# Kernel tuning notes

Hardware: AMD Instinct MI355X
Metric: run time of the kernel (lower is better)

## Reference

```python
import jax, jax.numpy as jnp
import numpy as np

# Tiny fixed contraction dims: M=3^(r_1-k), K=3^k, N=3^(r_2-k) with r_1=r_2=2, k=1
M, K, N = 3, 3, 3
R_O = 2  # output tensor rank -> output trailing shape (3,)*R_O == (3,3)


def setup_inputs() -> dict:
    key = jax.random.key(0)
    k1, k2 = jax.random.split(key)
    P, B, C = 4, 8192, 128
    T1 = jax.random.normal(k1, (P, B, C, M, K), dtype=jnp.float32)
    T2 = jax.random.normal(k2, (1, B, C, K, N), dtype=jnp.float32)
    return {"T1": T1, "T2": T2}


def reference(T1, T2):
    P, B, C = T1.shape[:3]
    T1m = T1.reshape(P, B, C, M, K)
    # T2 has a broadcast path dim of size 1; drop it and broadcast via einsum
    T2m = T2.reshape(B, C, K, N)
    out = jnp.einsum('pbcik,bckj->pbcij', T1m, T2m)
    return out.reshape((P, B, C) + (3,) * R_O)
```

## Files before the change

### kernel.cpp

```cpp
#include <hip/hip_runtime.h>


typedef float floatx4 __attribute__((ext_vector_type(4)));

__global__ __launch_bounds__(256) void tc33_kernel(const float* __restrict__ T1,
                                                   const float* __restrict__ T2,
                                                   float* __restrict__ out) {
    __shared__ float so[2304];
    const long long PER_P = 9LL * 8192 * 128;
    const int tid = threadIdx.x;
    const int w = tid >> 6;
    const int l = tid & 63;
    const long long cell  = (long long)blockIdx.x * 256 + tid;
    const long long cbase = cell * 9;
    const long long wbase = (long long)blockIdx.x * 2304 + (long long)w * 576;

    float* slice = so + w * 576;
    floatx4* S4  = reinterpret_cast<floatx4*>(slice);

    float b[9];
    {
        floatx4 v0 = *reinterpret_cast<const floatx4*>(T2 + cbase);
        floatx4 v1 = *reinterpret_cast<const floatx4*>(T2 + cbase + 4);
        float   v8 = T2[cbase + 8];
        b[0] = v0.x; b[1] = v0.y; b[2] = v0.z; b[3] = v0.w;
        b[4] = v1.x; b[5] = v1.y; b[6] = v1.z; b[7] = v1.w;
        b[8] = v8;
    }

    floatx4 ra0 = *reinterpret_cast<const floatx4*>(T1 + cbase);
    floatx4 ra1 = *reinterpret_cast<const floatx4*>(T1 + cbase + 4);
    float   ra8 = T1[cbase + 8];

    #pragma unroll
    for (int p = 0; p < 4; ++p) {
        float a[9];
        a[0] = ra0.x; a[1] = ra0.y; a[2] = ra0.z; a[3] = ra0.w;
        a[4] = ra1.x; a[5] = ra1.y; a[6] = ra1.z; a[7] = ra1.w;
        a[8] = ra8;

        if (p < 3) {
            const float* An = T1 + (long long)(p + 1) * PER_P + cbase;
            ra0 = *reinterpret_cast<const floatx4*>(An);
            ra1 = *reinterpret_cast<const floatx4*>(An + 4);
            ra8 = An[8];
        }

        float o[9];
        #pragma unroll
        for (int i = 0; i < 3; ++i) {
            #pragma unroll
            for (int j = 0; j < 3; ++j) {
                float s = a[i * 3 + 0] * b[0 * 3 + j];
                s = fmaf(a[i * 3 + 1], b[1 * 3 + j], s);
                s = fmaf(a[i * 3 + 2], b[2 * 3 + j], s);
                o[i * 3 + j] = s;
            }
        }

        #pragma unroll
        for (int i = 0; i < 9; ++i) slice[l * 9 + i] = o[i];

        __builtin_amdgcn_wave_barrier();

        floatx4 s0 = S4[l];
        floatx4 s1 = S4[l + 64];
        floatx4 s2;
        if (l < 16) s2 = S4[l + 128];

        floatx4* O4 = reinterpret_cast<floatx4*>(out + (long long)p * PER_P + wbase);
        O4[l]      = s0;
        O4[l + 64] = s1;
        if (l < 16) O4[l + 128] = s2;

        __builtin_amdgcn_wave_barrier();
    }
}

extern "C" void kernel_launch(void* const* d_in, const int* in_sizes, int n_in,
                              void* d_out, int out_size, void* d_ws, size_t ws_size,
                              hipStream_t stream) {
    const float* T1 = (const float*)d_in[0];
    const float* T2 = (const float*)d_in[1];
    float* out = (float*)d_out;

    const int threads = 256;
    const int blocks = (8192 * 128) / 256;
    tc33_kernel<<<blocks, threads, 0, stream>>>(T1, T2, out);
}
```

Before: 280.7 us.

## Split path dimension across blocks instead of looping per thread

Each block now handles one (p, chunk) pair, so the grid grows from 4096 to 16384 blocks and the per-thread loop over the four path slices goes away. This gives more parallelism and more memory requests in flight with less serial work per thread. The cost is that T2 is read four times, once per path block, rather than once, though repeated reads may hit in L2 or the last-level cache. The software prefetch of the next T1 slice is also dropped.

```diff
diff --git a/kernel.cpp b/kernel.cpp
--- a/kernel.cpp
+++ b/kernel.cpp
@@ -11,70 +11,58 @@
     const int tid = threadIdx.x;
     const int w = tid >> 6;
     const int l = tid & 63;
-    const long long cell  = (long long)blockIdx.x * 256 + tid;
-    const long long cbase = cell * 9;
-    const long long wbase = (long long)blockIdx.x * 2304 + (long long)w * 576;
+    const int bid = blockIdx.x;
+    const int p = bid >> 12;
+    const int chunk = bid & 4095;
+    const long long chunkBase = (long long)chunk * 2304;
+    const long long cbase = chunkBase + tid * 9;
+    const long long abase = (long long)p * PER_P + cbase;
+    const long long wbase = (long long)p * PER_P + chunkBase + (long long)w * 576;
 
     float* slice = so + w * 576;
     floatx4* S4  = reinterpret_cast<floatx4*>(slice);
 
-    float b[9];
-    {
-        floatx4 v0 = *reinterpret_cast<const floatx4*>(T2 + cbase);
-        floatx4 v1 = *reinterpret_cast<const floatx4*>(T2 + cbase + 4);
-        float   v8 = T2[cbase + 8];
-        b[0] = v0.x; b[1] = v0.y; b[2] = v0.z; b[3] = v0.w;
-        b[4] = v1.x; b[5] = v1.y; b[6] = v1.z; b[7] = v1.w;
-        b[8] = v8;
+    floatx4 vb0 = *reinterpret_cast<const floatx4*>(T2 + cbase);
+    floatx4 vb1 = *reinterpret_cast<const floatx4*>(T2 + cbase + 4);
+    float   vb8 = T2[cbase + 8];
+    floatx4 va0 = *reinterpret_cast<const floatx4*>(T1 + abase);
+    floatx4 va1 = *reinterpret_cast<const floatx4*>(T1 + abase + 4);
+    float   va8 = T1[abase + 8];
+
+    float b[9], a[9];
+    b[0] = vb0.x; b[1] = vb0.y; b[2] = vb0.z; b[3] = vb0.w;
+    b[4] = vb1.x; b[5] = vb1.y; b[6] = vb1.z; b[7] = vb1.w;
+    b[8] = vb8;
+    a[0] = va0.x; a[1] = va0.y; a[2] = va0.z; a[3] = va0.w;
+    a[4] = va1.x; a[5] = va1.y; a[6] = va1.z; a[7] = va1.w;
+    a[8] = va8;
+
+    float o[9];
+    #pragma unroll
+    for (int i = 0; i < 3; ++i) {
+        #pragma unroll
+        for (int j = 0; j < 3; ++j) {
+            float s = a[i * 3 + 0] * b[0 * 3 + j];
+            s = fmaf(a[i * 3 + 1], b[1 * 3 + j], s);
+            s = fmaf(a[i * 3 + 2], b[2 * 3 + j], s);
+            o[i * 3 + j] = s;
+        }
     }
 
-    floatx4 ra0 = *reinterpret_cast<const floatx4*>(T1 + cbase);
-    floatx4 ra1 = *reinterpret_cast<const floatx4*>(T1 + cbase + 4);
-    float   ra8 = T1[cbase + 8];
+    #pragma unroll
+    for (int i = 0; i < 9; ++i) slice[l * 9 + i] = o[i];
 
-    #pragma unroll
-    for (int p = 0; p < 4; ++p) {
-        float a[9];
-        a[0] = ra0.x; a[1] = ra0.y; a[2] = ra0.z; a[3] = ra0.w;
-        a[4] = ra1.x; a[5] = ra1.y; a[6] = ra1.z; a[7] = ra1.w;
-        a[8] = ra8;
+    __builtin_amdgcn_wave_barrier();
 
-        if (p < 3) {
-            const float* An = T1 + (long long)(p + 1) * PER_P + cbase;
-            ra0 = *reinterpret_cast<const floatx4*>(An);
-            ra1 = *reinterpret_cast<const floatx4*>(An + 4);
-            ra8 = An[8];
-        }
+    floatx4 s0 = S4[l];
+    floatx4 s1 = S4[l + 64];
+    floatx4 s2;
+    if (l < 16) s2 = S4[l + 128];
 
-        float o[9];
-        #pragma unroll
-        for (int i = 0; i < 3; ++i) {
-            #pragma unroll
-            for (int j = 0; j < 3; ++j) {
-                float s = a[i * 3 + 0] * b[0 * 3 + j];
-                s = fmaf(a[i * 3 + 1], b[1 * 3 + j], s);
-                s = fmaf(a[i * 3 + 2], b[2 * 3 + j], s);
-                o[i * 3 + j] = s;
-            }
-        }
-
-        #pragma unroll
-        for (int i = 0; i < 9; ++i) slice[l * 9 + i] = o[i];
-
-        __builtin_amdgcn_wave_barrier();
-
-        floatx4 s0 = S4[l];
-        floatx4 s1 = S4[l + 64];
-        floatx4 s2;
-        if (l < 16) s2 = S4[l + 128];
-
-        floatx4* O4 = reinterpret_cast<floatx4*>(out + (long long)p * PER_P + wbase);
-        O4[l]      = s0;
-        O4[l + 64] = s1;
-        if (l < 16) O4[l + 128] = s2;
-
-        __builtin_amdgcn_wave_barrier();
-    }
+    floatx4* O4 = reinterpret_cast<floatx4*>(out + wbase);
+    O4[l]      = s0;
+    O4[l + 64] = s1;
+    if (l < 16) O4[l + 128] = s2;
 }
 
 extern "C" void kernel_launch(void* const* d_in, const int* in_sizes, int n_in,
@@ -85,6 +73,6 @@
     float* out = (float*)d_out;
 
     const int threads = 256;
-    const int blocks = (8192 * 128) / 256;
+    const int blocks = 4 * 4096;
     tc33_kernel<<<blocks, threads, 0, stream>>>(T1, T2, out);
 }
```

Measured after the change: 277.4 us. Within noise of the previous version (-1.2%).
